# Performance work log

Hardware: AMD Instinct MI355X
Metric: run time of the kernel (lower is better)

## Reference

```python
import jax, jax.numpy as jnp
from jax import lax
import numpy as np

S = 2        # scale_factor
K = 5        # upsample_kernel_size
M = 64       # m_channels
C_IN = 128

def setup_inputs() -> dict:
    key = jax.random.key(0)
    k1, k2, k3, k4, k5 = jax.random.split(key, 5)
    B, C, H, W = 8, C_IN, 64, 64
    x = jax.random.normal(k1, (B, C, H, W), dtype=jnp.float32)
    compress_w = jax.random.normal(k2, (M, C, 1, 1), dtype=jnp.float32) * 0.05
    compress_b = jax.random.normal(k3, (M,), dtype=jnp.float32) * 0.05
    n_out = K * K * S * S  # 100
    encoder_w = jax.random.normal(k4, (n_out, M, 3, 3), dtype=jnp.float32) * 0.05
    encoder_b = jax.random.normal(k5, (n_out,), dtype=jnp.float32) * 0.05
    return {"x": x, "compress_w": compress_w, "compress_b": compress_b,
            "encoder_w": encoder_w, "encoder_b": encoder_b}

def _carafe(x, compress_w, compress_b, encoder_w, encoder_b):
    B, C, H, W = x.shape
    k, s = K, S
    nH, nW = s * H, s * W
    # 1x1 compress conv
    m = jnp.einsum('bchw,mc->bmhw', x, compress_w[:, :, 0, 0]) + compress_b[None, :, None, None]
    # 3x3 encoder conv, stride 1, pad 1 (SAME)
    ker = lax.conv_general_dilated(m, encoder_w, window_strides=(1, 1), padding='SAME',
                                   dimension_numbers=('NCHW', 'OIHW', 'NCHW'))
    ker = ker + encoder_b[None, :, None, None]  # (B, k*k*s*s, H, W)
    # PixelShuffle(s): (B, k*k, s, s, H, W) -> (B, k*k, H, s, W, s) -> (B, k*k, nH, nW)
    ker = ker.reshape(B, k * k, s, s, H, W).transpose(0, 1, 4, 2, 5, 3).reshape(B, k * k, nH, nW)
    ker = jax.nn.softmax(ker, axis=1)
    # Unfold(k, stride=1, pad=k//2): stack k*k shifted views, ordering (kh outer, kw inner)
    pad = k // 2
    xp = jnp.pad(x, ((0, 0), (0, 0), (pad, pad), (pad, pad)))
    patches = jnp.stack([xp[:, :, i:i + H, j:j + W] for i in range(k) for j in range(k)],
                        axis=2)  # (B, C, k*k, H, W)
    # nearest upsample by s on spatial dims
    up = jnp.repeat(jnp.repeat(patches, s, axis=3), s, axis=4)  # (B, C, k*k, nH, nW)
    # weighted local sum
    out = jnp.sum(up * ker[:, None, :, :, :], axis=2)  # (B, C, nH, nW)
    return out

def reference(x, compress_w, compress_b, encoder_w, encoder_b):
    return _carafe(x, compress_w, compress_b, encoder_w, encoder_b)
```

## Files before the change

### kernel.cpp

```cpp
#include <hip/hip_runtime.h>
#include <math.h>


typedef __attribute__((ext_vector_type(8))) short short8;
typedef __attribute__((ext_vector_type(4))) float floatx4;
typedef __attribute__((ext_vector_type(2))) float v2f;

__device__ __forceinline__ unsigned short f2bf(float f) {
  union { float f; unsigned int u; } v; v.f = f;
  unsigned int u = v.u + 0x7fffu + ((v.u >> 16) & 1u);
  return (unsigned short)(u >> 16);
}
__device__ __forceinline__ void unpack2(unsigned int u, float& lo, float& hi) {
  union { unsigned int u; float f; } a, b;
  a.u = u << 16; b.u = u & 0xffff0000u;
  lo = a.f; hi = b.f;
}
__device__ __forceinline__ v2f unpack2v(unsigned int u) {
  union { unsigned int u; float f; } a, b;
  a.u = u << 16; b.u = u & 0xffff0000u;
  return (v2f){a.f, b.f};
}

__global__ __launch_bounds__(256) void k_prep_pad(
    const float* __restrict__ x, const float* __restrict__ ew,
    const float* __restrict__ cw, unsigned short* __restrict__ a_prep,
    float* __restrict__ cwT, unsigned short* __restrict__ xpad) {
  const int blk = blockIdx.x;
  if (blk < 1024) {
    const float* xs = x + (size_t)blk * 4096;
    unsigned short* xd = xpad + (size_t)blk * 4896;
    for (int idx = threadIdx.x; idx < 1224; idx += 256) {
      int hp = idx / 18;
      int q = idx - hp * 18;
      int hh = hp - 2;
      int w0 = q * 4 - 2;
      float v0, v1, v2, v3;
      if (hh >= 0 && hh < 64 && w0 >= 0 && w0 + 3 < 64) {
        float4 xv = *(const float4*)&xs[hh * 64 + w0];
        v0 = xv.x; v1 = xv.y; v2 = xv.z; v3 = xv.w;
      } else {
        int base = hh * 64;
        bool hok = (hh >= 0 && hh < 64);
        v0 = (hok && w0 + 0 >= 0 && w0 + 0 < 64) ? xs[base + w0 + 0] : 0.f;
        v1 = (hok && w0 + 1 >= 0 && w0 + 1 < 64) ? xs[base + w0 + 1] : 0.f;
        v2 = (hok && w0 + 2 >= 0 && w0 + 2 < 64) ? xs[base + w0 + 2] : 0.f;
        v3 = (hok && w0 + 3 >= 0 && w0 + 3 < 64) ? xs[base + w0 + 3] : 0.f;
      }
      ushort4 o;
      o.x = f2bf(v0); o.y = f2bf(v1); o.z = f2bf(v2); o.w = f2bf(v3);
      *(ushort4*)&xd[idx * 4] = o;
    }
  } else {
    int idx = (blk - 1024) * 256 + (int)threadIdx.x;
    if (idx < 9 * 128 * 64) {
      int mo = idx & 63;
      int n = (idx >> 6) & 127;
      int tap = idx >> 13;
      float v = (n < 100) ? ew[(n * 64 + mo) * 9 + tap] : 0.f;
      a_prep[idx] = f2bf(v);
    } else {
      int r = idx - 9 * 128 * 64;
      int c = r >> 6, mo = r & 63;
      cwT[c * 64 + mo] = cw[mo * 128 + c];
    }
  }
}

__global__ __launch_bounds__(256) void k_compress(
    const float* __restrict__ x, const float* __restrict__ cwT,
    const float* __restrict__ cb, unsigned short* __restrict__ m_t) {
  __shared__ __align__(16) unsigned short ms[64][72];
  const int b = blockIdx.x >> 6;
  const int h = blockIdx.x & 63;
  const int wv = __builtin_amdgcn_readfirstlane((int)(threadIdx.x >> 6));
  const int lane = (int)(threadIdx.x & 63);
  const int mo0 = wv * 16;

  float acc[16];
#pragma unroll
  for (int k = 0; k < 16; ++k) acc[k] = 0.f;

  const float* xp = x + (((size_t)b * 128) * 64 + h) * 64 + lane;
  const float* wp = cwT + mo0;

#pragma unroll 4
  for (int c = 0; c < 128; ++c) {
    float xv = xp[(size_t)c * 4096];
#pragma unroll
    for (int k = 0; k < 16; ++k)
      acc[k] = fmaf(xv, wp[c * 64 + k], acc[k]);
  }

#pragma unroll
  for (int k = 0; k < 16; ++k) acc[k] += cb[mo0 + k];

#pragma unroll
  for (int k = 0; k < 8; ++k) {
    unsigned int p = ((unsigned int)f2bf(acc[2 * k + 1]) << 16) | f2bf(acc[2 * k]);
    *(unsigned int*)&ms[lane][mo0 + 2 * k] = p;
  }
  __syncthreads();
  const int t = threadIdx.x;
#pragma unroll
  for (int rep = 0; rep < 2; ++rep) {
    int idx = t + rep * 256;
    uint4 v = *(const uint4*)&ms[idx >> 3][(idx & 7) * 8];
    *(uint4*)&m_t[(size_t)blockIdx.x * 4096 + idx * 8] = v;
  }
}

__global__ __launch_bounds__(256) void k_main(
    const unsigned short* __restrict__ m_t, const unsigned short* __restrict__ a_prep,
    const float* __restrict__ eb, const unsigned short* __restrict__ xpad,
    float* __restrict__ out) {
  __shared__ __align__(16) float raw[128 * 66];
  unsigned short* m_s = (unsigned short*)raw;
  unsigned short* wgt_s = (unsigned short*)raw;
  const int b = blockIdx.x >> 6;
  const int h = blockIdx.x & 63;
  const int t = threadIdx.x;

  for (int idx = t; idx < 3 * 64 * 8; idx += 256) {
    int r = idx >> 9;
    int rem = idx & 511;
    int w = rem >> 3, u = rem & 7;
    int hh = h + r - 1;
    uint4 val = make_uint4(0u, 0u, 0u, 0u);
    if (hh >= 0 && hh < 64)
      val = *(const uint4*)&m_t[(((b * 64 + hh) * 64 + w) * 64) + u * 8];
    *(uint4*)&m_s[(r * 64 + w) * 72 + u * 8] = val;
  }
  __syncthreads();

  const int wave = t >> 6, lane = t & 63;
  const int quad = lane >> 4, col = lane & 15;
  const int nbase = wave * 32;

  const floatx4 z4 = {0.f, 0.f, 0.f, 0.f};
  floatx4 acc[2][4];
#pragma unroll
  for (int i = 0; i < 2; ++i)
#pragma unroll
    for (int p = 0; p < 4; ++p) acc[i][p] = z4;

  const short8 z8 = {0, 0, 0, 0, 0, 0, 0, 0};

#pragma unroll
  for (int tap = 0; tap < 9; ++tap) {
    const int dh = tap / 3, dw = tap % 3;
#pragma unroll
    for (int half = 0; half < 2; ++half) {
      const int mo0 = half * 32;
      short8 a0 = *(const short8*)&a_prep[((tap * 128 + nbase + col) * 64) + mo0 + quad * 8];
      short8 a1 = *(const short8*)&a_prep[((tap * 128 + nbase + 16 + col) * 64) + mo0 + quad * 8];
#pragma unroll
      for (int p = 0; p < 4; ++p) {
        int wsrc = p * 16 + col + dw - 1;
        int wc = min(max(wsrc, 0), 63);
        short8 bf = *(const short8*)&m_s[(dh * 64 + wc) * 72 + mo0 + quad * 8];
        if (wsrc < 0 || wsrc > 63) bf = z8;
        acc[0][p] = __builtin_amdgcn_mfma_f32_16x16x32_bf16(a0, bf, acc[0][p], 0, 0, 0);
        acc[1][p] = __builtin_amdgcn_mfma_f32_16x16x32_bf16(a1, bf, acc[1][p], 0, 0, 0);
      }
    }
  }

  __syncthreads();
#pragma unroll
  for (int i = 0; i < 2; ++i)
#pragma unroll
    for (int p = 0; p < 4; ++p)
#pragma unroll
      for (int r = 0; r < 4; ++r)
        raw[(nbase + i * 16 + quad * 4 + r) * 66 + p * 16 + col] = acc[i][p][r];
  __syncthreads();

  const int q = wave;
  float v[25];
  float mx = -1e30f;
#pragma unroll
  for (int kk = 0; kk < 25; ++kk) {
    v[kk] = raw[(kk * 4 + q) * 66 + lane] + eb[kk * 4 + q];
    mx = fmaxf(mx, v[kk]);
  }
  float s = 0.f;
#pragma unroll
  for (int kk = 0; kk < 25; ++kk) {
    v[kk] = __expf(v[kk] - mx);
    s += v[kk];
  }
  float inv = 1.f / s;

  __syncthreads();
  {
    const int ohl = q >> 1;
    const int owp = 2 * lane + (q & 1);
#pragma unroll
    for (int kk = 0; kk < 25; ++kk)
      wgt_s[(ohl * 25 + kk) * 128 + owp] = f2bf(v[kk] * inv);
  }
  __syncthreads();

  const int wg = t & 15;
  const int cg = t >> 4;
  const int w0 = wg * 4;

  for (int chalf = 0; chalf < 2; ++chalf) {
    const int c0 = chalf * 64 + cg * 4;
    const unsigned short* xb =
        xpad + ((size_t)(b * 128 + c0) * 4896) + h * 72 + w0;

    v2f accB[2][4][4];
#pragma unroll
    for (int oh = 0; oh < 2; ++oh)
#pragma unroll
      for (int ch = 0; ch < 4; ++ch)
#pragma unroll
        for (int k = 0; k < 4; ++k) accB[oh][ch][k] = (v2f){0.f, 0.f};

    for (int i = 0; i < 5; ++i) {
      float xr[4][8];
#pragma unroll
      for (int ch = 0; ch < 4; ++ch) {
        uint4 rawv = *(const uint4*)(xb + ch * 4896 + i * 72);
        unpack2(rawv.x, xr[ch][0], xr[ch][1]);
        unpack2(rawv.y, xr[ch][2], xr[ch][3]);
        unpack2(rawv.z, xr[ch][4], xr[ch][5]);
        unpack2(rawv.w, xr[ch][6], xr[ch][7]);
      }
#pragma unroll
      for (int j = 0; j < 5; ++j) {
        const int ij = i * 5 + j;
#pragma unroll
        for (int oh = 0; oh < 2; ++oh) {
          uint4 wr = *(const uint4*)&wgt_s[(oh * 25 + ij) * 128 + w0 * 2];
          v2f wp[4];
          wp[0] = unpack2v(wr.x);
          wp[1] = unpack2v(wr.y);
          wp[2] = unpack2v(wr.z);
          wp[3] = unpack2v(wr.w);
#pragma unroll
          for (int k = 0; k < 4; ++k)
#pragma unroll
            for (int ch = 0; ch < 4; ++ch) {
              float xv = xr[ch][k + j];
              v2f xvv = {xv, xv};
              accB[oh][ch][k] += xvv * wp[k];
            }
        }
      }
    }

#pragma unroll
    for (int ch = 0; ch < 4; ++ch)
#pragma unroll
      for (int oh = 0; oh < 2; ++oh) {
        float* orow =
            out + ((size_t)(b * 128 + c0 + ch) * 128 + (2 * h + oh)) * 128 + w0 * 2;
        float4 f0 = make_float4(accB[oh][ch][0].x, accB[oh][ch][0].y,
                                accB[oh][ch][1].x, accB[oh][ch][1].y);
        float4 f1 = make_float4(accB[oh][ch][2].x, accB[oh][ch][2].y,
                                accB[oh][ch][3].x, accB[oh][ch][3].y);
        *(float4*)orow = f0;
        *(float4*)(orow + 4) = f1;
      }
  }
}

extern "C" void kernel_launch(void* const* d_in, const int* in_sizes, int n_in,
                              void* d_out, int out_size, void* d_ws, size_t ws_size,
                              hipStream_t stream) {
  (void)in_sizes; (void)n_in; (void)out_size; (void)ws_size;
  const float* x  = (const float*)d_in[0];
  const float* cw = (const float*)d_in[1];
  const float* cb = (const float*)d_in[2];
  const float* ew = (const float*)d_in[3];
  const float* eb = (const float*)d_in[4];
  float* out = (float*)d_out;

  char* wsb = (char*)d_ws;
  unsigned short* m_t    = (unsigned short*)(wsb);
  unsigned short* a_prep = (unsigned short*)(wsb + 4194304);
  unsigned short* xpad   = (unsigned short*)(wsb + 4341760);
  float*          cwT    = (float*)(wsb + 14368768);

  k_prep_pad<<<dim3(1344), dim3(256), 0, stream>>>(x, ew, cw, a_prep, cwT, xpad);
  k_compress<<<dim3(512), dim3(256), 0, stream>>>(x, cwT, cb, m_t);
  k_main<<<dim3(512), dim3(256), 0, stream>>>(m_t, a_prep, eb, xpad, out);
}
```

Baseline: 144.9 us.

## Fuse bf16 padded-x conversion into compress kernel and swizzle block order

The conversion of x to a padded bf16 buffer moves out of the prep kernel and into the compress kernel. The compress kernel now stages each x row through shared memory, writing both the fp32 copy used for the 1x1 conv and the bf16 padded interior, so x is read from global memory only once. The prep kernel now only zeroes the pad borders. Block indices in the compress and main kernels are also remapped (interleaving batches) so that concurrently running blocks touch different batches, in exchange for a larger shared footprint and uncoalesced 2-byte stores into xpad.

```diff
diff --git a/kernel.cpp b/kernel.cpp
--- a/kernel.cpp
+++ b/kernel.cpp
@@ -22,37 +22,13 @@
   return (v2f){a.f, b.f};
 }
 
-__global__ __launch_bounds__(256) void k_prep_pad(
-    const float* __restrict__ x, const float* __restrict__ ew,
-    const float* __restrict__ cw, unsigned short* __restrict__ a_prep,
-    float* __restrict__ cwT, unsigned short* __restrict__ xpad) {
+__global__ __launch_bounds__(256) void k_prep(
+    const float* __restrict__ ew, const float* __restrict__ cw,
+    unsigned short* __restrict__ a_prep, float* __restrict__ cwT,
+    unsigned short* __restrict__ xpad) {
   const int blk = blockIdx.x;
-  if (blk < 1024) {
-    const float* xs = x + (size_t)blk * 4096;
-    unsigned short* xd = xpad + (size_t)blk * 4896;
-    for (int idx = threadIdx.x; idx < 1224; idx += 256) {
-      int hp = idx / 18;
-      int q = idx - hp * 18;
-      int hh = hp - 2;
-      int w0 = q * 4 - 2;
-      float v0, v1, v2, v3;
-      if (hh >= 0 && hh < 64 && w0 >= 0 && w0 + 3 < 64) {
-        float4 xv = *(const float4*)&xs[hh * 64 + w0];
-        v0 = xv.x; v1 = xv.y; v2 = xv.z; v3 = xv.w;
-      } else {
-        int base = hh * 64;
-        bool hok = (hh >= 0 && hh < 64);
-        v0 = (hok && w0 + 0 >= 0 && w0 + 0 < 64) ? xs[base + w0 + 0] : 0.f;
-        v1 = (hok && w0 + 1 >= 0 && w0 + 1 < 64) ? xs[base + w0 + 1] : 0.f;
-        v2 = (hok && w0 + 2 >= 0 && w0 + 2 < 64) ? xs[base + w0 + 2] : 0.f;
-        v3 = (hok && w0 + 3 >= 0 && w0 + 3 < 64) ? xs[base + w0 + 3] : 0.f;
-      }
-      ushort4 o;
-      o.x = f2bf(v0); o.y = f2bf(v1); o.z = f2bf(v2); o.w = f2bf(v3);
-      *(ushort4*)&xd[idx * 4] = o;
-    }
-  } else {
-    int idx = (blk - 1024) * 256 + (int)threadIdx.x;
+  if (blk < 320) {
+    int idx = blk * 256 + (int)threadIdx.x;
     if (idx < 9 * 128 * 64) {
       int mo = idx & 63;
       int n = (idx >> 6) & 127;
@@ -64,29 +40,63 @@
       int c = r >> 6, mo = r & 63;
       cwT[c * 64 + mo] = cw[mo * 128 + c];
     }
-  }
-}
-
-__global__ __launch_bounds__(256) void k_compress(
+  } else {
+    int local = blk - 320;
+    for (int i = threadIdx.x; i < 800; i += 256) {
+      int which = (i >= 400);
+      int k = i - which * 400;
+      unsigned int* pd =
+          (unsigned int*)(xpad + (size_t)(local * 2 + which) * 4896);
+      int u32idx;
+      if (k < 72) {
+        u32idx = k;
+      } else if (k < 144) {
+        u32idx = 2376 + (k - 72);
+      } else {
+        int j = k - 144;
+        int r = 2 + (j >> 2), s = j & 3;
+        u32idx = r * 36 + (s ? 32 + s : 0);
+      }
+      pd[u32idx] = 0u;
+    }
+  }
+}
+
+__global__ __launch_bounds__(256) void k_comp_pad(
     const float* __restrict__ x, const float* __restrict__ cwT,
-    const float* __restrict__ cb, unsigned short* __restrict__ m_t) {
-  __shared__ __align__(16) unsigned short ms[64][72];
-  const int b = blockIdx.x >> 6;
-  const int h = blockIdx.x & 63;
-  const int wv = __builtin_amdgcn_readfirstlane((int)(threadIdx.x >> 6));
-  const int lane = (int)(threadIdx.x & 63);
+    const float* __restrict__ cb, unsigned short* __restrict__ m_t,
+    unsigned short* __restrict__ xpad) {
+  __shared__ __align__(16) float xs[128 * 64];
+  const int lb = (((int)blockIdx.x & 7) << 6) | ((int)blockIdx.x >> 3);
+  const int b = lb >> 6;
+  const int h = lb & 63;
+  const int t = (int)threadIdx.x;
+
+  const float* xrow = x + (((size_t)b * 128) * 64 + h) * 64;
+  unsigned short* xpd = xpad + (size_t)b * 128 * 4896 + (h + 2) * 72 + 2;
+#pragma unroll
+  for (int it = 0; it < 32; ++it) {
+    int idx = it * 256 + t;
+    int c = idx >> 6, w = idx & 63;
+    float v = xrow[(size_t)c * 4096 + w];
+    xs[idx] = v;
+    xpd[(size_t)c * 4896 + w] = f2bf(v);
+  }
+  __syncthreads();
+
+  const int wv = __builtin_amdgcn_readfirstlane(t >> 6);
+  const int lane = t & 63;
   const int mo0 = wv * 16;
 
   float acc[16];
 #pragma unroll
   for (int k = 0; k < 16; ++k) acc[k] = 0.f;
 
-  const float* xp = x + (((size_t)b * 128) * 64 + h) * 64 + lane;
   const float* wp = cwT + mo0;
 
 #pragma unroll 4
   for (int c = 0; c < 128; ++c) {
-    float xv = xp[(size_t)c * 4096];
+    float xv = xs[c * 64 + lane];
 #pragma unroll
     for (int k = 0; k < 16; ++k)
       acc[k] = fmaf(xv, wp[c * 64 + k], acc[k]);
@@ -95,18 +105,19 @@
 #pragma unroll
   for (int k = 0; k < 16; ++k) acc[k] += cb[mo0 + k];
 
+  __syncthreads();
+  unsigned short* ms = (unsigned short*)xs;
 #pragma unroll
   for (int k = 0; k < 8; ++k) {
     unsigned int p = ((unsigned int)f2bf(acc[2 * k + 1]) << 16) | f2bf(acc[2 * k]);
-    *(unsigned int*)&ms[lane][mo0 + 2 * k] = p;
-  }
-  __syncthreads();
-  const int t = threadIdx.x;
+    *(unsigned int*)&ms[lane * 72 + mo0 + 2 * k] = p;
+  }
+  __syncthreads();
 #pragma unroll
   for (int rep = 0; rep < 2; ++rep) {
     int idx = t + rep * 256;
-    uint4 v = *(const uint4*)&ms[idx >> 3][(idx & 7) * 8];
-    *(uint4*)&m_t[(size_t)blockIdx.x * 4096 + idx * 8] = v;
+    uint4 v = *(const uint4*)&ms[(idx >> 3) * 72 + (idx & 7) * 8];
+    *(uint4*)&m_t[(size_t)lb * 4096 + idx * 8] = v;
   }
 }
 
@@ -117,9 +128,10 @@
   __shared__ __align__(16) float raw[128 * 66];
   unsigned short* m_s = (unsigned short*)raw;
   unsigned short* wgt_s = (unsigned short*)raw;
-  const int b = blockIdx.x >> 6;
-  const int h = blockIdx.x & 63;
-  const int t = threadIdx.x;
+  const int lb = (((int)blockIdx.x & 7) << 6) | ((int)blockIdx.x >> 3);
+  const int b = lb >> 6;
+  const int h = lb & 63;
+  const int t = (int)threadIdx.x;
 
   for (int idx = t; idx < 3 * 64 * 8; idx += 256) {
     int r = idx >> 9;
@@ -285,7 +297,7 @@
   unsigned short* xpad   = (unsigned short*)(wsb + 4341760);
   float*          cwT    = (float*)(wsb + 14368768);
 
-  k_prep_pad<<<dim3(1344), dim3(256), 0, stream>>>(x, ew, cw, a_prep, cwT, xpad);
-  k_compress<<<dim3(512), dim3(256), 0, stream>>>(x, cwT, cb, m_t);
+  k_prep<<<dim3(832), dim3(256), 0, stream>>>(ew, cw, a_prep, cwT, xpad);
+  k_comp_pad<<<dim3(512), dim3(256), 0, stream>>>(x, cwT, cb, m_t, xpad);
   k_main<<<dim3(512), dim3(256), 0, stream>>>(m_t, a_prep, eb, xpad, out);
 }
```

Measured after the change: 134.7 us, median of 3. 1.08x faster.
